# Kernel optimization log

Measured on AMD Instinct MI355X. Metric: run time of the kernel, lower is better.

## Reference

```python
import jax, jax.numpy as jnp
import numpy as np

B, T, C, D = 256, 128, 141, 1536  # batch, tokens, max chars, feature dim
H = 141                            # lstm hidden
G = 4 * H                          # gate dim
L = 4                              # lstm layers


def setup_inputs() -> dict:
    key = jax.random.key(0)
    ks = jax.random.split(key, 20)
    s = 0.05
    tok_feats = jax.random.normal(ks[0], (B, T, D), jnp.float32)
    # non-overlapping char spans per token, clipped to C (some zero-length)
    lens = jax.random.randint(ks[1], (B, T), 0, 3)
    ends = jnp.cumsum(lens, axis=1)
    starts = ends - lens
    offset_mapping = jnp.stack([jnp.minimum(starts, C), jnp.minimum(ends, C)], axis=-1).astype(jnp.int32)
    return {
        "tok_feats": tok_feats,
        "offset_mapping": offset_mapping,
        "h0": jnp.zeros((2 * L, B, H), jnp.float32),
        "c0": jnp.zeros((2 * L, B, H), jnp.float32),
        "w_lin": jax.random.normal(ks[2], (D, D), jnp.float32) * s,
        "b_lin": jnp.zeros((D,), jnp.float32),
        "w_ih0_f": jax.random.normal(ks[3], (G, D), jnp.float32) * s,
        "w_ih0_b": jax.random.normal(ks[4], (G, D), jnp.float32) * s,
        "w_ih_f": jax.random.normal(ks[5], (L - 1, G, 2 * H), jnp.float32) * s,
        "w_ih_b": jax.random.normal(ks[6], (L - 1, G, 2 * H), jnp.float32) * s,
        "w_hh_f": jax.random.normal(ks[7], (L, G, H), jnp.float32) * s,
        "w_hh_b": jax.random.normal(ks[8], (L, G, H), jnp.float32) * s,
        "b_f": jnp.zeros((L, G), jnp.float32),
        "b_b": jnp.zeros((L, G), jnp.float32),
        "w1": jax.random.normal(ks[9], (2 * H, 2 * H), jnp.float32) * s,
        "b1": jnp.zeros((2 * H,), jnp.float32),
        "w2": jax.random.normal(ks[10], (2, 2 * H), jnp.float32) * s,
        "b2": jnp.zeros((2,), jnp.float32),
    }


def _scatter_chars(X, offset_mapping):
    # Vectorized equivalent of: for each token, write its vector into chars [start,end)
    starts = offset_mapping[..., 0]  # [B,T]
    ends = offset_mapping[..., 1]
    c = jnp.arange(C)
    cover = (starts[:, :, None] <= c) & (c < ends[:, :, None])  # [B,T,C]
    tok_idx = jnp.argmax(cover, axis=1)                          # [B,C]
    has = jnp.any(cover, axis=1)                                 # [B,C]
    chars = jnp.take_along_axis(X, tok_idx[:, :, None], axis=1)  # [B,C,D]
    return jnp.where(has[:, :, None], chars, jnp.zeros((), X.dtype))


def _run_dir(x, h_init, c_init, w_ih, w_hh, b, reverse):
    # x: [B,S,in]; precompute input contribution [S,B,4H]
    xW = jnp.swapaxes(jnp.einsum('bsd,gd->bsg', x, w_ih) + b, 0, 1)

    def step(carry, xt):
        h, cc = carry
        g = xt + h @ w_hh.T
        i = jax.nn.sigmoid(g[:, :H])
        f = jax.nn.sigmoid(g[:, H:2 * H])
        gg = jnp.tanh(g[:, 2 * H:3 * H])
        o = jax.nn.sigmoid(g[:, 3 * H:])
        c2 = f * cc + i * gg
        h2 = o * jnp.tanh(c2)
        return (h2, c2), h2

    (hn, cn), ys = jax.lax.scan(step, (h_init, c_init), xW, reverse=reverse)
    return jnp.swapaxes(ys, 0, 1), hn, cn  # [B,S,H]


def reference(tok_feats, offset_mapping, h0, c0, w_lin, b_lin,
              w_ih0_f, w_ih0_b, w_ih_f, w_ih_b, w_hh_f, w_hh_b, b_f, b_b,
              w1, b1, w2, b2):
    X = tok_feats @ w_lin.T + b_lin            # token-level linear (dropout is identity at eval)
    x = _scatter_chars(X, offset_mapping)      # [B,141,1536]
    h_list, c_list = [], []
    for l in range(L):
        wi_f = w_ih0_f if l == 0 else w_ih_f[l - 1]
        wi_b = w_ih0_b if l == 0 else w_ih_b[l - 1]
        out_f, hf, cf = _run_dir(x, h0[2 * l], c0[2 * l], wi_f, w_hh_f[l], b_f[l], False)
        out_b, hb, cb = _run_dir(x, h0[2 * l + 1], c0[2 * l + 1], wi_b, w_hh_b[l], b_b[l], True)
        x = jnp.concatenate([out_f, out_b], axis=-1)  # [B,141,282]
        h_list += [hf, hb]
        c_list += [cf, cb]
    hn = jnp.stack(h_list)
    cn = jnp.stack(c_list)
    y = x @ w1.T + b1
    y = y @ w2.T + b2                          # [B,141,2]
    X1, X2 = y[..., :1], y[..., 1:]
    return (X1, X2, hn, cn)
```

## Files before the change

kernel.cpp:

```cpp
#include <hip/hip_runtime.h>
#include <hip/hip_bf16.h>

#define Bb 256
#define Tt 128
#define Cc 141
#define Dd 1536
#define Hh 141
#define Gg 564
#define Gp 576
#define Nc 1152
#define K2p 320
#define MM (Bb*Cc)

typedef float f32x4 __attribute__((ext_vector_type(4)));
typedef short s16x8 __attribute__((ext_vector_type(8)));
typedef _Float16 h2 __attribute__((ext_vector_type(2)));

typedef __attribute__((address_space(1))) const void GvT;
typedef __attribute__((address_space(3))) void LvT;
#define GLOAD16(g, l) __builtin_amdgcn_global_load_lds((GvT*)(g), (LvT*)(l), 16, 0, 0)

__device__ __forceinline__ short f2bf(float f){
    union { float f; unsigned u; } v; v.f = f;
    unsigned r = v.u + 0x7fffu + ((v.u >> 16) & 1u);
    return (short)(r >> 16);
}
__device__ __forceinline__ float bf2f(short s){
    union { unsigned u; float f; } v; v.u = ((unsigned)(unsigned short)s) << 16;
    return v.f;
}
__device__ __forceinline__ float fdot2(h2 a, h2 b, float c){
#if __has_builtin(__builtin_amdgcn_fdot2)
    return __builtin_amdgcn_fdot2(a, b, c, false);
#else
    return c + (float)a.x * (float)b.x + (float)a.y * (float)b.y;
#endif
}
__device__ __forceinline__ float sigm(float x){ return 1.f / (1.f + __expf(-x)); }
__device__ __forceinline__ float tanh_(float x){ float e = __expf(2.f * x); return 1.f - 2.f / (e + 1.f); }

__global__ __launch_bounds__(256) void convert_pad(const float* __restrict__ src,
                                                   short* __restrict__ dst,
                                                   int R, int Kin, int Rp, int Kp){
    int idx = blockIdx.x * 256 + threadIdx.x;
    if (idx >= Rp * Kp) return;
    int r = idx / Kp, k = idx - r * Kp;
    float v = (r < R && k < Kin) ? src[(size_t)r * Kin + k] : 0.f;
    dst[idx] = f2bf(v);
}

__global__ __launch_bounds__(256) void build_gather(const int* __restrict__ offm,
                                                    int* __restrict__ gidx){
    int m = blockIdx.x * 256 + threadIdx.x;
    if (m >= MM) return;
    int b = m / Cc, c = m - b * Cc;
    int found = -1;
    for (int t = 0; t < Tt; t++){
        int s = offm[((size_t)(b * Tt + t)) * 2];
        int e = offm[((size_t)(b * Tt + t)) * 2 + 1];
        if (s <= c && c < e){ found = b * Tt + t; break; }
    }
    gidx[m] = found;
}

__global__ __launch_bounds__(256) void gather_convert(const float* __restrict__ tok,
                                                      const int* __restrict__ gidx,
                                                      short* __restrict__ xg){
    size_t idx = (size_t)blockIdx.x * 256 + threadIdx.x;
    if (idx >= (size_t)MM * 192) return;
    int m = (int)(idx / 192), c8 = (int)(idx % 192);
    int g = gidx[m];
    s16x8 o = (s16x8)0;
    if (g >= 0){
        const float* s = tok + (size_t)g * Dd + c8 * 8;
        float4 v0 = *(const float4*)s;
        float4 v1 = *(const float4*)(s + 4);
        o[0] = f2bf(v0.x); o[1] = f2bf(v0.y); o[2] = f2bf(v0.z); o[3] = f2bf(v0.w);
        o[4] = f2bf(v1.x); o[5] = f2bf(v1.y); o[6] = f2bf(v1.z); o[7] = f2bf(v1.w);
    }
    *(s16x8*)(xg + (size_t)m * Dd + c8 * 8) = o;
}

__global__ __launch_bounds__(256, 2) void gemm128(const short* __restrict__ A,
                                                  const short* __restrict__ Bw,
                                                  const float* __restrict__ bias1,
                                                  const float* __restrict__ bias2,
                                                  int nb1, int nb2, int halfN,
                                                  short* __restrict__ Cout,
                                                  const int* __restrict__ gidx,
                                                  int K, int NT, int ldc){
    __shared__ short As[128 * 64];
    __shared__ short Bs[128 * 64];
    const int nwg = gridDim.x;
    const int id = blockIdx.x;
    const int q = nwg >> 3, r = nwg & 7;
    const int xcd = id & 7, pos = id >> 3;
    const int wg = (xcd < r ? xcd * (q + 1) : r * (q + 1) + (xcd - r) * q) + pos;
    const int m0 = (wg / NT) * 128, n0 = (wg % NT) * 128;
    const int tid = threadIdx.x, lane = tid & 63, wv = tid >> 6;
    const int wm = wv >> 1, wn = wv & 1;
    const int r16 = lane & 15, kq = lane >> 4;

    f32x4 acc[4][4] = {};

    for (int k0 = 0; k0 < K; k0 += 64){
        #pragma unroll
        for (int i = 0; i < 4; i++){
            int e = (i * 4 + wv) * 64 + lane;
            int row = e >> 3, ch = e & 7;
            int sc = ch ^ (row & 7);
            GLOAD16(A + (size_t)(m0 + row) * K + k0 + (sc << 3),
                    As + (i * 4 + wv) * 512);
        }
        #pragma unroll
        for (int i = 0; i < 4; i++){
            int e = (i * 4 + wv) * 64 + lane;
            int row = e >> 3, ch = e & 7;
            int sc = ch ^ (row & 7);
            GLOAD16(Bw + (size_t)(n0 + row) * K + k0 + (sc << 3),
                    Bs + (i * 4 + wv) * 512);
        }
        __syncthreads();
        #pragma unroll
        for (int ks = 0; ks < 2; ks++){
            s16x8 af[4], bfr[4];
            #pragma unroll
            for (int mt = 0; mt < 4; mt++){
                int row = wm * 64 + mt * 16 + r16;
                int c = (ks * 4 + kq) ^ (row & 7);
                af[mt] = *(const s16x8*)(As + row * 64 + (c << 3));
            }
            #pragma unroll
            for (int nt = 0; nt < 4; nt++){
                int row = wn * 64 + nt * 16 + r16;
                int c = (ks * 4 + kq) ^ (row & 7);
                bfr[nt] = *(const s16x8*)(Bs + row * 64 + (c << 3));
            }
            #pragma unroll
            for (int mt = 0; mt < 4; mt++)
                #pragma unroll
                for (int nt = 0; nt < 4; nt++)
                    acc[mt][nt] = __builtin_amdgcn_mfma_f32_16x16x32_bf16(af[mt], bfr[nt], acc[mt][nt], 0, 0, 0);
        }
        __syncthreads();
    }

    #pragma unroll
    for (int nt = 0; nt < 4; nt++){
        int col = n0 + wn * 64 + nt * 16 + r16;
        float bv;
        if (col < halfN) bv = (col < nb1) ? bias1[col] : 0.f;
        else             bv = (col - halfN < nb2) ? bias2[col - halfN] : 0.f;
        #pragma unroll
        for (int mt = 0; mt < 4; mt++){
            int rowb = m0 + wm * 64 + mt * 16 + kq * 4;
            #pragma unroll
            for (int rr = 0; rr < 4; rr++){
                int row = rowb + rr;
                float v = acc[mt][nt][rr] + bv;
                if (gidx && gidx[row] < 0) v = 0.f;
                Cout[(size_t)row * ldc + col] = f2bf(v);
            }
        }
    }
}

__global__ __launch_bounds__(576, 4) void lstm_scan(const short* __restrict__ xW,
                                                    const float* __restrict__ whh_f,
                                                    const float* __restrict__ whh_b,
                                                    const float* __restrict__ h0l,
                                                    const float* __restrict__ c0l,
                                                    short* __restrict__ xout,
                                                    float* __restrict__ hnl,
                                                    float* __restrict__ cnl){
    const int dir = blockIdx.x & 1;
    const int b = blockIdx.x >> 1;
    const int j = threadIdx.x;
    const float* whh = dir ? whh_b : whh_f;

    __shared__ float pre[Gg];
    __shared__ h2 hsh[72];

    h2 wreg[71];
    if (j < Gg){
        const float* wr = whh + (size_t)j * Hh;
        #pragma unroll
        for (int kk = 0; kk < 70; kk++){
            h2 w; w.x = (_Float16)wr[2 * kk]; w.y = (_Float16)wr[2 * kk + 1];
            wreg[kk] = w;
        }
        h2 w; w.x = (_Float16)wr[140]; w.y = (_Float16)0.f;
        wreg[70] = w;
    }

    float hcur = 0.f, ccur = 0.f;
    if (j < Hh){
        hcur = h0l[(size_t)dir * Bb * Hh + b * Hh + j];
        ccur = c0l[(size_t)dir * Bb * Hh + b * Hh + j];
    }
    if (j < 144) ((_Float16*)hsh)[j] = (j < Hh) ? (_Float16)hcur : (_Float16)0.f;
    __syncthreads();

    const short* xcol = xW + (size_t)b * Cc * Nc + dir * Gp + j;
    const int dt = dir ? -1 : 1;

    short xwraw = 0;
    if (j < Gg) xwraw = xcol[(size_t)(dir ? (Cc - 1) : 0) * Nc];

    for (int t = 0; t < Cc; t++){
        int tt = dir ? (Cc - 1 - t) : t;
        short xwraw_n = 0;
        if (t + 1 < Cc && j < Gg) xwraw_n = xcol[(size_t)(tt + dt) * Nc];

        if (j < Gg){
            float acc0 = 0.f, acc1 = 0.f;
            #pragma unroll
            for (int kk = 0; kk < 71; kk++){
                if (kk & 1) acc1 = fdot2(wreg[kk], hsh[kk], acc1);
                else        acc0 = fdot2(wreg[kk], hsh[kk], acc0);
            }
            pre[j] = bf2f(xwraw) + acc0 + acc1;
        }
        asm volatile("s_waitcnt lgkmcnt(0)" ::: "memory");
        __builtin_amdgcn_s_barrier();
        if (j < Hh){
            float gi = sigm(pre[j]);
            float gf = sigm(pre[j + Hh]);
            float gg = tanh_(pre[j + 2 * Hh]);
            float go = sigm(pre[j + 3 * Hh]);
            ccur = gf * ccur + gi * gg;
            hcur = go * tanh_(ccur);
            xout[((size_t)b * Cc + tt) * K2p + dir * Hh + j] = f2bf(hcur);
            ((_Float16*)hsh)[j] = (_Float16)hcur;
        }
        asm volatile("s_waitcnt lgkmcnt(0)" ::: "memory");
        __builtin_amdgcn_s_barrier();
        xwraw = xwraw_n;
    }
    if (j < Hh){
        hnl[(size_t)dir * Bb * Hh + b * Hh + j] = hcur;
        cnl[(size_t)dir * Bb * Hh + b * Hh + j] = ccur;
    }
}

__global__ __launch_bounds__(384) void wc_build(const float* __restrict__ w1,
                                                const float* __restrict__ b1,
                                                const float* __restrict__ w2,
                                                const float* __restrict__ b2,
                                                float* __restrict__ Wc){
    int j = threadIdx.x;
    if (j < K2p){
        float a0 = 0.f, a1 = 0.f;
        if (j < 282){
            for (int k = 0; k < 282; k++){
                float w = w1[(size_t)k * 282 + j];
                a0 += w2[k] * w;
                a1 += w2[282 + k] * w;
            }
        }
        Wc[j] = a0;
        Wc[K2p + j] = a1;
    } else if (j < K2p + 2){
        int o = j - K2p;
        float s = b2[o];
        for (int k = 0; k < 282; k++) s += w2[(size_t)o * 282 + k] * b1[k];
        Wc[2 * K2p + o] = s;
    }
}

__global__ __launch_bounds__(256) void head2_k(const short* __restrict__ x4,
                                               const float* __restrict__ Wc,
                                               float* __restrict__ X1,
                                               float* __restrict__ X2){
    int m = blockIdx.x * 256 + threadIdx.x;
    if (m >= MM) return;
    const short* xr = x4 + (size_t)m * K2p;
    float a0 = 0.f, a1 = 0.f;
    #pragma unroll 4
    for (int c = 0; c < 36; c++){
        s16x8 v = *(const s16x8*)(xr + c * 8);
        #pragma unroll
        for (int u = 0; u < 8; u++){
            float xv = bf2f(v[u]);
            a0 += xv * Wc[c * 8 + u];
            a1 += xv * Wc[K2p + c * 8 + u];
        }
    }
    X1[m] = a0 + Wc[2 * K2p];
    X2[m] = a1 + Wc[2 * K2p + 1];
}

extern "C" void kernel_launch(void* const* d_in, const int* in_sizes, int n_in,
                              void* d_out, int out_size, void* d_ws, size_t ws_size,
                              hipStream_t stream){
    const float* tok     = (const float*)d_in[0];
    const int*   offm    = (const int*)d_in[1];
    const float* h0      = (const float*)d_in[2];
    const float* c0      = (const float*)d_in[3];
    const float* w_lin   = (const float*)d_in[4];
    const float* b_lin   = (const float*)d_in[5];
    const float* w_ih0_f = (const float*)d_in[6];
    const float* w_ih0_b = (const float*)d_in[7];
    const float* w_ih_f  = (const float*)d_in[8];
    const float* w_ih_b  = (const float*)d_in[9];
    const float* w_hh_f  = (const float*)d_in[10];
    const float* w_hh_b  = (const float*)d_in[11];
    const float* b_f     = (const float*)d_in[12];
    const float* b_b     = (const float*)d_in[13];
    const float* w1      = (const float*)d_in[14];
    const float* b1      = (const float*)d_in[15];
    const float* w2      = (const float*)d_in[16];
    const float* b2      = (const float*)d_in[17];

    float* out = (float*)d_out;
    float* oX1 = out;
    float* oX2 = out + MM;
    float* ohn = out + 2 * MM;
    float* ocn = ohn + 8 * Bb * Hh;

    char* ws = (char*)d_ws;
    size_t off = 0;
    auto alloc = [&](size_t bytes) -> void* {
        void* p = ws + off;
        off += (bytes + 255) & ~(size_t)255;
        return p;
    };
    short* region1 = (short*)alloc((size_t)MM * Dd * 2);
    short* region2 = (short*)alloc((size_t)MM * Dd * 2);
    short* wlin16  = (short*)alloc((size_t)Dd * Dd * 2);
    short* w0c     = (short*)alloc((size_t)Nc * Dd * 2);
    short* wc123   = (short*)alloc((size_t)3 * Nc * K2p * 2);
    int*   gidx    = (int*)alloc((size_t)MM * 4);
    float* Wc      = (float*)alloc((size_t)(2 * K2p + 2) * 4);

    short* xg = region1;
    short* xW = region1;
    short* x0 = region2;
    short* xA = region2;
    short* xB = region2 + (size_t)MM * K2p;

    auto cdiv = [](int a, int b){ return (a + b - 1) / b; };

    convert_pad<<<cdiv(Dd * Dd, 256), 256, 0, stream>>>(w_lin, wlin16, Dd, Dd, Dd, Dd);
    convert_pad<<<cdiv(Gp * Dd, 256), 256, 0, stream>>>(w_ih0_f, w0c, Gg, Dd, Gp, Dd);
    convert_pad<<<cdiv(Gp * Dd, 256), 256, 0, stream>>>(w_ih0_b, w0c + (size_t)Gp * Dd, Gg, Dd, Gp, Dd);
    for (int l = 1; l < 4; l++){
        short* wl = wc123 + (size_t)(l - 1) * Nc * K2p;
        convert_pad<<<cdiv(Gp * K2p, 256), 256, 0, stream>>>(w_ih_f + (size_t)(l - 1) * Gg * 282,
                                                             wl, Gg, 282, Gp, K2p);
        convert_pad<<<cdiv(Gp * K2p, 256), 256, 0, stream>>>(w_ih_b + (size_t)(l - 1) * Gg * 282,
                                                             wl + (size_t)Gp * K2p, Gg, 282, Gp, K2p);
    }
    wc_build<<<1, 384, 0, stream>>>(w1, b1, w2, b2, Wc);

    build_gather<<<cdiv(MM, 256), 256, 0, stream>>>(offm, gidx);
    gather_convert<<<cdiv(MM * 192, 256), 256, 0, stream>>>(tok, gidx, xg);

    gemm128<<<282 * (Dd / 128), 256, 0, stream>>>(xg, wlin16, b_lin, b_lin,
                                                  Dd, 0, Dd, x0, gidx, Dd, Dd / 128, Dd);

    const short* xin = x0;
    int Kl = Dd;
    short* outbuf[4] = { xA, xB, xA, xB };
    for (int l = 0; l < 4; l++){
        const short* wl = (l == 0) ? w0c : wc123 + (size_t)(l - 1) * Nc * K2p;
        gemm128<<<282 * (Nc / 128), 256, 0, stream>>>(xin, wl,
                                                      b_f + (size_t)l * Gg, b_b + (size_t)l * Gg,
                                                      Gg, Gg, Gp, xW, nullptr, Kl, Nc / 128, Nc);
        lstm_scan<<<512, 576, 0, stream>>>(xW,
                                           w_hh_f + (size_t)l * Gg * Hh, w_hh_b + (size_t)l * Gg * Hh,
                                           h0 + (size_t)(2 * l) * Bb * Hh, c0 + (size_t)(2 * l) * Bb * Hh,
                                           outbuf[l],
                                           ohn + (size_t)(2 * l) * Bb * Hh, ocn + (size_t)(2 * l) * Bb * Hh);
        xin = outbuf[l];
        Kl = K2p;
    }

    head2_k<<<cdiv(MM, 256), 256, 0, stream>>>(xB, Wc, oX1, oX2);
}
```

Before: 2.252 ms.

## Halve LSTM scan block size, two gate rows per thread with vectorized h loads

The recurrent scan kernel now runs 288 threads per block instead of 576, and each active thread holds two rows of the recurrent weights (j and j+282) in registers as fp16 pairs. The hidden state is read from shared memory as 8-wide fp16 vectors and reused across both rows. This halves the LDS reads of h per gate and reduces barrier cost, since fewer waves join each barrier. In exchange each thread needs about 144 packed registers for weights, which lowers occupancy, and the per-thread dot-product chain becomes twice as long.

```diff
diff --git a/kernel.cpp b/kernel.cpp
--- a/kernel.cpp
+++ b/kernel.cpp
@@ -15,6 +15,7 @@
 typedef float f32x4 __attribute__((ext_vector_type(4)));
 typedef short s16x8 __attribute__((ext_vector_type(8)));
 typedef _Float16 h2 __attribute__((ext_vector_type(2)));
+typedef _Float16 h8 __attribute__((ext_vector_type(8)));
 
 typedef __attribute__((address_space(1))) const void GvT;
 typedef __attribute__((address_space(3))) void LvT;
@@ -165,32 +166,35 @@
     }
 }
 
-__global__ __launch_bounds__(576, 4) void lstm_scan(const short* __restrict__ xW,
-                                                    const float* __restrict__ whh_f,
-                                                    const float* __restrict__ whh_b,
-                                                    const float* __restrict__ h0l,
-                                                    const float* __restrict__ c0l,
-                                                    short* __restrict__ xout,
-                                                    float* __restrict__ hnl,
-                                                    float* __restrict__ cnl){
+__global__ __launch_bounds__(288) __attribute__((amdgpu_waves_per_eu(1, 3)))
+void lstm_scan(const short* __restrict__ xW,
+               const float* __restrict__ whh_f,
+               const float* __restrict__ whh_b,
+               const float* __restrict__ h0l,
+               const float* __restrict__ c0l,
+               short* __restrict__ xout,
+               float* __restrict__ hnl,
+               float* __restrict__ cnl){
     const int dir = blockIdx.x & 1;
     const int b = blockIdx.x >> 1;
     const int j = threadIdx.x;
     const float* whh = dir ? whh_b : whh_f;
 
     __shared__ float pre[Gg];
-    __shared__ h2 hsh[72];
-
-    h2 wreg[71];
-    if (j < Gg){
-        const float* wr = whh + (size_t)j * Hh;
+    __shared__ h8 hsh8[18];
+
+    h2 wreg[144];
+    if (j < 282){
+        const float* wa = whh + (size_t)j * Hh;
+        const float* wb = whh + (size_t)(j + 282) * Hh;
         #pragma unroll
         for (int kk = 0; kk < 70; kk++){
-            h2 w; w.x = (_Float16)wr[2 * kk]; w.y = (_Float16)wr[2 * kk + 1];
-            wreg[kk] = w;
-        }
-        h2 w; w.x = (_Float16)wr[140]; w.y = (_Float16)0.f;
-        wreg[70] = w;
+            h2 a; a.x = (_Float16)wa[2*kk]; a.y = (_Float16)wa[2*kk+1]; wreg[kk] = a;
+            h2 c; c.x = (_Float16)wb[2*kk]; c.y = (_Float16)wb[2*kk+1]; wreg[72+kk] = c;
+        }
+        h2 za; za.x = (_Float16)wa[140]; za.y = (_Float16)0.f; wreg[70] = za;
+        h2 zb; zb.x = (_Float16)wb[140]; zb.y = (_Float16)0.f; wreg[142] = zb;
+        h2 z; z.x = (_Float16)0.f; z.y = (_Float16)0.f; wreg[71] = z; wreg[143] = z;
     }
 
     float hcur = 0.f, ccur = 0.f;
@@ -198,28 +202,42 @@
         hcur = h0l[(size_t)dir * Bb * Hh + b * Hh + j];
         ccur = c0l[(size_t)dir * Bb * Hh + b * Hh + j];
     }
-    if (j < 144) ((_Float16*)hsh)[j] = (j < Hh) ? (_Float16)hcur : (_Float16)0.f;
+    if (j < 144) ((_Float16*)hsh8)[j] = (j < Hh) ? (_Float16)hcur : (_Float16)0.f;
     __syncthreads();
 
-    const short* xcol = xW + (size_t)b * Cc * Nc + dir * Gp + j;
+    const short* xc = xW + (size_t)b * Cc * Nc + dir * Gp + j;
     const int dt = dir ? -1 : 1;
-
-    short xwraw = 0;
-    if (j < Gg) xwraw = xcol[(size_t)(dir ? (Cc - 1) : 0) * Nc];
+    const int t0 = dir ? (Cc - 1) : 0;
+
+    short xwA = 0, xwB = 0;
+    if (j < 282){
+        xwA = xc[(size_t)t0 * Nc];
+        xwB = xc[(size_t)t0 * Nc + 282];
+    }
 
     for (int t = 0; t < Cc; t++){
         int tt = dir ? (Cc - 1 - t) : t;
-        short xwraw_n = 0;
-        if (t + 1 < Cc && j < Gg) xwraw_n = xcol[(size_t)(tt + dt) * Nc];
-
-        if (j < Gg){
-            float acc0 = 0.f, acc1 = 0.f;
-            #pragma unroll
-            for (int kk = 0; kk < 71; kk++){
-                if (kk & 1) acc1 = fdot2(wreg[kk], hsh[kk], acc1);
-                else        acc0 = fdot2(wreg[kk], hsh[kk], acc0);
-            }
-            pre[j] = bf2f(xwraw) + acc0 + acc1;
+        short nA = 0, nB = 0;
+        if (t + 1 < Cc && j < 282){
+            nA = xc[(size_t)(tt + dt) * Nc];
+            nB = xc[(size_t)(tt + dt) * Nc + 282];
+        }
+
+        if (j < 282){
+            float a0 = 0.f, a1 = 0.f, b0 = 0.f, b1 = 0.f;
+            #pragma unroll
+            for (int c = 0; c < 18; c++){
+                h8 hv = hsh8[c];
+                h2* ph = (h2*)&hv;
+                #pragma unroll
+                for (int u = 0; u < 4; u++){
+                    int kk = c * 4 + u;
+                    if (u & 1){ a1 = fdot2(wreg[kk], ph[u], a1); b1 = fdot2(wreg[72+kk], ph[u], b1); }
+                    else      { a0 = fdot2(wreg[kk], ph[u], a0); b0 = fdot2(wreg[72+kk], ph[u], b0); }
+                }
+            }
+            pre[j]       = bf2f(xwA) + a0 + a1;
+            pre[j + 282] = bf2f(xwB) + b0 + b1;
         }
         asm volatile("s_waitcnt lgkmcnt(0)" ::: "memory");
         __builtin_amdgcn_s_barrier();
@@ -231,11 +249,11 @@
             ccur = gf * ccur + gi * gg;
             hcur = go * tanh_(ccur);
             xout[((size_t)b * Cc + tt) * K2p + dir * Hh + j] = f2bf(hcur);
-            ((_Float16*)hsh)[j] = (_Float16)hcur;
+            ((_Float16*)hsh8)[j] = (_Float16)hcur;
         }
         asm volatile("s_waitcnt lgkmcnt(0)" ::: "memory");
         __builtin_amdgcn_s_barrier();
-        xwraw = xwraw_n;
+        xwA = nA; xwB = nB;
     }
     if (j < Hh){
         hnl[(size_t)dir * Bb * Hh + b * Hh + j] = hcur;
@@ -367,7 +385,7 @@
         gemm128<<<282 * (Nc / 128), 256, 0, stream>>>(xin, wl,
                                                       b_f + (size_t)l * Gg, b_b + (size_t)l * Gg,
                                                       Gg, Gg, Gp, xW, nullptr, Kl, Nc / 128, Nc);
-        lstm_scan<<<512, 576, 0, stream>>>(xW,
+        lstm_scan<<<512, 288, 0, stream>>>(xW,
                                            w_hh_f + (size_t)l * Gg * Hh, w_hh_b + (size_t)l * Gg * Hh,
                                            h0 + (size_t)(2 * l) * Bb * Hh, c0 + (size_t)(2 * l) * Bb * Hh,
                                            outbuf[l],
```

New measurement: 2.173 ms. 3.5% less time.
